# Kernel optimization log

Hardware: AMD Instinct MI355X
Metric: run time of the kernel (lower is better)

## Reference

```python
import jax, jax.numpy as jnp
import numpy as np

B, A, T, D = 4, 64, 128, 512
H = 8
DH = D // H
DFF = 4 * D

def layer_norm(x, g, b, eps=1e-5):
    mu = jnp.mean(x, axis=-1, keepdims=True)
    var = jnp.var(x, axis=-1, keepdims=True)
    return (x - mu) * jax.lax.rsqrt(var + eps) * g + b

def setup_inputs() -> dict:
    key = jax.random.key(0)
    ks = jax.random.split(key, 8)
    s = 0.02
    return {
        "x": jax.random.normal(ks[0], (B, A, T, D), dtype=jnp.float32),
        "ln1_g": jnp.ones((D,), jnp.float32),
        "ln1_b": jnp.zeros((D,), jnp.float32),
        "W_qkv": jax.random.normal(ks[1], (D, 3 * D), jnp.float32) * s,
        "b_qkv": jnp.zeros((3 * D,), jnp.float32),
        "W_proj": jax.random.normal(ks[2], (D, D), jnp.float32) * s,
        "b_proj": jnp.zeros((D,), jnp.float32),
        "ln2_g": jnp.ones((D,), jnp.float32),
        "ln2_b": jnp.zeros((D,), jnp.float32),
        "W_fc": jax.random.normal(ks[3], (D, DFF), jnp.float32) * s,
        "b_fc": jnp.zeros((DFF,), jnp.float32),
        "W_out": jax.random.normal(ks[4], (DFF, D), jnp.float32) * s,
        "b_out": jnp.zeros((D,), jnp.float32),
    }

def reference(x, ln1_g, ln1_b, W_qkv, b_qkv, W_proj, b_proj,
              ln2_g, ln2_b, W_fc, b_fc, W_out, b_out):
    # pre-norm (note: original adds residual from the NORMED x)
    xn = layer_norm(x, ln1_g, ln1_b)
    # qkv projection: [B,A,T,3D]
    qkv = xn @ W_qkv + b_qkv
    q, k, v = jnp.split(qkv, 3, axis=-1)
    # [B,A,T,H,DH]
    q = q.reshape(B, A, T, H, DH)
    k = k.reshape(B, A, T, H, DH)
    v = v.reshape(B, A, T, H, DH)
    # attention across time, per (batch, agent, head): scores [B,A,H,T,T]
    att = jnp.einsum('bathd,bashd->bahts', q, k) * (1.0 / np.sqrt(DH))
    causal = jnp.tril(jnp.ones((T, T), dtype=bool))
    att = jnp.where(causal, att, -jnp.inf)
    att = jax.nn.softmax(att, axis=-1)
    y = jnp.einsum('bahts,bashd->bathd', att, v).reshape(B, A, T, D)
    y = y @ W_proj + b_proj
    x = xn + y
    # MLP block
    xn2 = layer_norm(x, ln2_g, ln2_b)
    h = jax.nn.gelu(xn2 @ W_fc + b_fc, approximate=False)
    m = h @ W_out + b_out
    return xn2 + m
```

## Files before the change

### kernel.cpp

```cpp
#include <hip/hip_runtime.h>
#include <math.h>

#define DEV static __device__ __forceinline__

typedef unsigned short u16;
typedef __attribute__((ext_vector_type(8))) short short8;
typedef __attribute__((ext_vector_type(4))) float floatx4;

DEV u16 f2bf(float f) {
  unsigned u = __float_as_uint(f);
  unsigned r = u + 0x7FFFu + ((u >> 16) & 1u);
  return (u16)(r >> 16);
}
DEV float bf2f(u16 v) { return __uint_as_float(((unsigned)v) << 16); }

typedef __attribute__((address_space(1))) void gvoid;
typedef __attribute__((address_space(3))) void lvoid;

DEV void gload16(const u16* g, u16* l) {
  __builtin_amdgcn_global_load_lds((gvoid*)g, (lvoid*)l, 16, 0, 0);
}

__global__ __launch_bounds__(256) void tcast_k(const float* __restrict__ in,
                                               u16* __restrict__ out, int K, int N) {
  __shared__ float t[32][33];
  int nb = blockIdx.x * 32, kb = blockIdx.y * 32;
  int tx = threadIdx.x, ty = threadIdx.y;
#pragma unroll
  for (int r = 0; r < 32; r += 8)
    t[r + ty][tx] = in[(long)(kb + r + ty) * N + nb + tx];
  __syncthreads();
#pragma unroll
  for (int r = 0; r < 32; r += 8)
    out[(long)(nb + r + ty) * K + kb + tx] = f2bf(t[tx][r + ty]);
}

template <typename TI>
__global__ __launch_bounds__(256) void ln_k(const TI* __restrict__ x,
                                            const float* __restrict__ g,
                                            const float* __restrict__ b,
                                            u16* __restrict__ xb) {
  const int lane = threadIdx.x & 63, wid = threadIdx.x >> 6;
  const long row = (long)blockIdx.x * 4 + wid;
  float vv[8];
  if constexpr (sizeof(TI) == 4) {
    const float4* xr = (const float4*)((const float*)x + row * 512);
    float4 v0 = xr[lane * 2], v1 = xr[lane * 2 + 1];
    vv[0] = v0.x; vv[1] = v0.y; vv[2] = v0.z; vv[3] = v0.w;
    vv[4] = v1.x; vv[5] = v1.y; vv[6] = v1.z; vv[7] = v1.w;
  } else {
    short8 v = *(const short8*)((const u16*)x + row * 512 + lane * 8);
#pragma unroll
    for (int i = 0; i < 8; ++i) vv[i] = bf2f((u16)v[i]);
  }
  float s = 0.f, q = 0.f;
#pragma unroll
  for (int i = 0; i < 8; ++i) { s += vv[i]; q += vv[i] * vv[i]; }
#pragma unroll
  for (int off = 1; off < 64; off <<= 1) {
    s += __shfl_xor(s, off, 64);
    q += __shfl_xor(q, off, 64);
  }
  float mean = s * (1.f / 512.f);
  float var = q * (1.f / 512.f) - mean * mean;
  float rs = rsqrtf(var + 1e-5f);
  const float4* gp = (const float4*)g;
  const float4* bp = (const float4*)b;
  float4 g0 = gp[lane * 2], g1 = gp[lane * 2 + 1];
  float4 b0 = bp[lane * 2], b1 = bp[lane * 2 + 1];
  float gg[8] = {g0.x, g0.y, g0.z, g0.w, g1.x, g1.y, g1.z, g1.w};
  float bb[8] = {b0.x, b0.y, b0.z, b0.w, b1.x, b1.y, b1.z, b1.w};
  short8 ov;
#pragma unroll
  for (int i = 0; i < 8; ++i)
    ov[i] = (short)f2bf((vv[i] - mean) * rs * gg[i] + bb[i]);
  *(short8*)&xb[row * 512 + lane * 8] = ov;
}

template <int EPI>
__global__ __launch_bounds__(256) void gemm_k(const u16* __restrict__ A,
                                              const u16* __restrict__ Bt,
                                              const float* __restrict__ bias,
                                              const u16* __restrict__ res,
                                              void* __restrict__ out,
                                              int M, int N, int K) {
  __shared__ __align__(16) u16 lA[128 * 32];
  __shared__ __align__(16) u16 lB[128 * 32];
  const int tid = threadIdx.x;
  const int lane = tid & 63, wid = tid >> 6;
  const int lane15 = lane & 15, khi = lane >> 4;
  const int wr = wid >> 1, wc = wid & 1;
  const long rowB = (long)blockIdx.y * 128;
  const long colB = (long)blockIdx.x * 128;

  floatx4 acc[4][4];
#pragma unroll
  for (int m = 0; m < 4; ++m)
#pragma unroll
    for (int n = 0; n < 4; ++n) acc[m][n] = floatx4{0.f, 0.f, 0.f, 0.f};

  for (int kt = 0; kt < K; kt += 32) {
    __syncthreads();
#pragma unroll
    for (int j = 0; j < 2; ++j) {
      int c = j * 256 + tid;
      int r = c >> 2, cq = c & 3;
      gload16(A + (rowB + r) * K + kt + cq * 8, &lA[(j * 256 + wid * 64) * 8]);
    }
#pragma unroll
    for (int j = 0; j < 2; ++j) {
      int c = j * 256 + tid;
      int r = c >> 2, cq = c & 3;
      gload16(Bt + (colB + r) * K + kt + cq * 8, &lB[(j * 256 + wid * 64) * 8]);
    }
    asm volatile("s_waitcnt vmcnt(0)" ::: "memory");
    __syncthreads();

    short8 af[4];
#pragma unroll
    for (int m = 0; m < 4; ++m)
      af[m] = *(const short8*)&lA[(wr * 64 + m * 16 + lane15) * 32 + khi * 8];
#pragma unroll
    for (int n = 0; n < 4; ++n) {
      short8 bfg = *(const short8*)&lB[(wc * 64 + n * 16 + lane15) * 32 + khi * 8];
#pragma unroll
      for (int m = 0; m < 4; ++m)
        acc[m][n] = __builtin_amdgcn_mfma_f32_16x16x32_bf16(af[m], bfg, acc[m][n], 0, 0, 0);
    }
  }

  const long r0 = rowB + wr * 64;
  const long c0 = colB + wc * 64;
#pragma unroll
  for (int m = 0; m < 4; ++m) {
#pragma unroll
    for (int n = 0; n < 4; ++n) {
      long col = c0 + n * 16 + lane15;
      float bv = bias[col];
#pragma unroll
      for (int jj = 0; jj < 4; ++jj) {
        long row = r0 + m * 16 + khi * 4 + jj;
        float v = acc[m][n][jj] + bv;
        if (EPI == 1) v = 0.5f * v * (1.f + erff(v * 0.70710678118f));
        if (EPI == 2 || EPI == 3) v += bf2f(res[row * N + col]);
        if (EPI == 3) {
          ((float*)out)[row * N + col] = v;
        } else {
          ((u16*)out)[row * N + col] = f2bf(v);
        }
      }
    }
  }
}

__global__ __launch_bounds__(256) void attn_k(const u16* __restrict__ qkv,
                                              u16* __restrict__ y) {
  union U {
    struct { u16 q[128 * 64]; u16 k[128 * 64]; } qk;
    u16 p[128 * 128];
  };
  __shared__ __align__(16) U u;
  __shared__ __align__(16) u16 vt[64 * 128];

  const int tid = threadIdx.x;
  const int lane = tid & 63, wid = tid >> 6;
  const int lane15 = lane & 15, khi = lane >> 4;
  const int h = blockIdx.x & 7;
  const long R0 = (long)(blockIdx.x >> 3) * 128;
  const u16* base = qkv + R0 * 1536 + h * 64;

#pragma unroll
  for (int it = 0; it < 4; ++it) {
    int c = it * 256 + tid;
    int r = c >> 3, ch = c & 7;
    const u16* gq = base + (long)r * 1536 + ch * 8;
    uint4 dq = *(const uint4*)gq;
    uint4 dk = *(const uint4*)(gq + 512);
    uint4 dv = *(const uint4*)(gq + 1024);
    int qi = (r * 64 + ch * 8) ^ ((r & 7) << 3);
    *(uint4*)&u.qk.q[qi] = dq;
    *(uint4*)&u.qk.k[qi] = dk;
    u16 tmp[8];
    *(uint4*)tmp = dv;
#pragma unroll
    for (int i = 0; i < 8; ++i) {
      int d = ch * 8 + i;
      vt[(d * 128 + r) ^ ((d & 7) << 3)] = tmp[i];
    }
  }
  __syncthreads();

  const int r0 = wid * 32;
  floatx4 sc[2][8];
#pragma unroll
  for (int mt = 0; mt < 2; ++mt)
#pragma unroll
    for (int c = 0; c < 8; ++c) sc[mt][c] = floatx4{0.f, 0.f, 0.f, 0.f};

#pragma unroll
  for (int kk = 0; kk < 2; ++kk) {
    short8 aq[2];
#pragma unroll
    for (int mt = 0; mt < 2; ++mt) {
      int rr = r0 + mt * 16 + lane15;
      aq[mt] = *(const short8*)&u.qk.q[(rr * 64 + kk * 32 + khi * 8) ^ ((rr & 7) << 3)];
    }
#pragma unroll
    for (int c = 0; c < 8; ++c) {
      int rk = c * 16 + lane15;
      short8 bk = *(const short8*)&u.qk.k[(rk * 64 + kk * 32 + khi * 8) ^ ((rk & 7) << 3)];
#pragma unroll
      for (int mt = 0; mt < 2; ++mt)
        sc[mt][c] = __builtin_amdgcn_mfma_f32_16x16x32_bf16(aq[mt], bk, sc[mt][c], 0, 0, 0);
    }
  }
  __syncthreads();

#pragma unroll
  for (int mt = 0; mt < 2; ++mt) {
#pragma unroll
    for (int jj = 0; jj < 4; ++jj) {
      int t = r0 + mt * 16 + khi * 4 + jj;
      float vals[8];
      float mx = -1e30f;
#pragma unroll
      for (int c = 0; c < 8; ++c) {
        int s = c * 16 + lane15;
        float v = sc[mt][c][jj] * 0.125f;
        vals[c] = (s <= t) ? v : -1e30f;
        mx = fmaxf(mx, vals[c]);
      }
#pragma unroll
      for (int off = 1; off < 16; off <<= 1) mx = fmaxf(mx, __shfl_xor(mx, off, 64));
      float sum = 0.f;
#pragma unroll
      for (int c = 0; c < 8; ++c) {
        float p = __expf(vals[c] - mx);
        vals[c] = p;
        sum += p;
      }
#pragma unroll
      for (int off = 1; off < 16; off <<= 1) sum += __shfl_xor(sum, off, 64);
      float inv = 1.f / sum;
#pragma unroll
      for (int c = 0; c < 8; ++c) {
        int s = c * 16 + lane15;
        u.p[(t * 128 + s) ^ ((t & 7) << 3)] = f2bf(vals[c] * inv);
      }
    }
  }
  __syncthreads();

  floatx4 ya[2][4];
#pragma unroll
  for (int mt = 0; mt < 2; ++mt)
#pragma unroll
    for (int n = 0; n < 4; ++n) ya[mt][n] = floatx4{0.f, 0.f, 0.f, 0.f};

#pragma unroll
  for (int kk = 0; kk < 4; ++kk) {
    short8 ap[2];
#pragma unroll
    for (int mt = 0; mt < 2; ++mt) {
      int rr = r0 + mt * 16 + lane15;
      ap[mt] = *(const short8*)&u.p[(rr * 128 + kk * 32 + khi * 8) ^ ((rr & 7) << 3)];
    }
#pragma unroll
    for (int n = 0; n < 4; ++n) {
      int d = n * 16 + lane15;
      short8 bv = *(const short8*)&vt[(d * 128 + kk * 32 + khi * 8) ^ ((d & 7) << 3)];
#pragma unroll
      for (int mt = 0; mt < 2; ++mt)
        ya[mt][n] = __builtin_amdgcn_mfma_f32_16x16x32_bf16(ap[mt], bv, ya[mt][n], 0, 0, 0);
    }
  }

  u16* yb = y + R0 * 512 + h * 64;
#pragma unroll
  for (int mt = 0; mt < 2; ++mt)
#pragma unroll
    for (int n = 0; n < 4; ++n)
#pragma unroll
      for (int jj = 0; jj < 4; ++jj) {
        int t = r0 + mt * 16 + khi * 4 + jj;
        int d = n * 16 + lane15;
        yb[(long)t * 512 + d] = f2bf(ya[mt][n][jj]);
      }
}

extern "C" void kernel_launch(void* const* d_in, const int* in_sizes, int n_in,
                              void* d_out, int out_size, void* d_ws, size_t ws_size,
                              hipStream_t stream) {
  const float* x      = (const float*)d_in[0];
  const float* ln1_g  = (const float*)d_in[1];
  const float* ln1_b  = (const float*)d_in[2];
  const float* W_qkv  = (const float*)d_in[3];
  const float* b_qkv  = (const float*)d_in[4];
  const float* W_proj = (const float*)d_in[5];
  const float* b_proj = (const float*)d_in[6];
  const float* ln2_g  = (const float*)d_in[7];
  const float* ln2_b  = (const float*)d_in[8];
  const float* W_fc   = (const float*)d_in[9];
  const float* b_fc   = (const float*)d_in[10];
  const float* W_out  = (const float*)d_in[11];
  const float* b_out  = (const float*)d_in[12];

  const size_t MiB = 1024 * 1024;
  char* ws = (char*)d_ws;
  u16* wq   = (u16*)(ws + 0);
  u16* wp   = (u16*)(ws + 1536 * 512 * 2);
  u16* wf   = (u16*)(ws + 2 * MiB);
  u16* wo   = (u16*)(ws + 4 * MiB);
  u16* xnB  = (u16*)(ws + 8 * MiB);
  u16* qkvB = (u16*)(ws + 40 * MiB);
  u16* yB   = (u16*)(ws + 136 * MiB);
  u16* x2B  = (u16*)(ws + 40 * MiB);
  u16* xn2B = (u16*)(ws + 8 * MiB);
  u16* hB   = (u16*)(ws + 40 * MiB);

  const int M = 32768;

  tcast_k<<<dim3(1536 / 32, 512 / 32), dim3(32, 8), 0, stream>>>(W_qkv, wq, 512, 1536);
  tcast_k<<<dim3(512 / 32, 512 / 32), dim3(32, 8), 0, stream>>>(W_proj, wp, 512, 512);
  tcast_k<<<dim3(2048 / 32, 512 / 32), dim3(32, 8), 0, stream>>>(W_fc, wf, 512, 2048);
  tcast_k<<<dim3(512 / 32, 2048 / 32), dim3(32, 8), 0, stream>>>(W_out, wo, 2048, 512);

  ln_k<float><<<M / 4, 256, 0, stream>>>(x, ln1_g, ln1_b, xnB);
  gemm_k<0><<<dim3(1536 / 128, M / 128), 256, 0, stream>>>(xnB, wq, b_qkv, nullptr,
                                                           qkvB, M, 1536, 512);
  attn_k<<<2048, 256, 0, stream>>>(qkvB, yB);
  gemm_k<2><<<dim3(512 / 128, M / 128), 256, 0, stream>>>(yB, wp, b_proj, xnB,
                                                          x2B, M, 512, 512);
  ln_k<u16><<<M / 4, 256, 0, stream>>>(x2B, ln2_g, ln2_b, xn2B);
  gemm_k<1><<<dim3(2048 / 128, M / 128), 256, 0, stream>>>(xn2B, wf, b_fc, nullptr,
                                                           hB, M, 2048, 512);
  gemm_k<3><<<dim3(512 / 128, M / 128), 256, 0, stream>>>(hB, wo, b_out, xn2B,
                                                          (float*)d_out, M, 512, 2048);
}
```

Baseline: 532.5 us.

## Fuse LN1 with QKV GEMM and proj+LN2+MLP into one row-block kernel

Replaces the separate layernorm and GEMM launches with two fused kernels. Each block owns 128 rows, holds the normalized activations in a 128 KB LDS tile and streams bf16 weights directly from global memory. In the second kernel, projection, residual, LN2, FC+GELU in 64-column chunks and the output GEMM all run without writing the intermediates x2, xn2 and h to HBM. The trade is that only 256 blocks of 512 threads run, with one block per CU because of the LDS footprint. Weight fragments are also loaded from global memory with no LDS staging or software pipelining, so latency hiding and occupancy may suffer.

```diff
diff --git a/kernel.cpp b/kernel.cpp
--- a/kernel.cpp
+++ b/kernel.cpp
@@ -20,6 +20,13 @@
 DEV void gload16(const u16* g, u16* l) {
   __builtin_amdgcn_global_load_lds((gvoid*)g, (lvoid*)l, 16, 0, 0);
 }
+
+DEV floatx4 mfma16(short8 a, short8 b, floatx4 c) {
+  return __builtin_amdgcn_mfma_f32_16x16x32_bf16(a, b, c, 0, 0, 0);
+}
+
+DEV int aidx(int r, int g) { return r * 512 + ((g ^ (r & 7)) << 3); }
+DEV int hidx(int r, int g) { return (r << 6) + ((g ^ (r & 7)) << 3); }
 
 __global__ __launch_bounds__(256) void tcast_k(const float* __restrict__ in,
                                                u16* __restrict__ out, int K, int N) {
@@ -35,121 +42,87 @@
     out[(long)(nb + r + ty) * K + kb + tx] = f2bf(t[tx][r + ty]);
 }
 
-template <typename TI>
-__global__ __launch_bounds__(256) void ln_k(const TI* __restrict__ x,
-                                            const float* __restrict__ g,
-                                            const float* __restrict__ b,
-                                            u16* __restrict__ xb) {
-  const int lane = threadIdx.x & 63, wid = threadIdx.x >> 6;
-  const long row = (long)blockIdx.x * 4 + wid;
-  float vv[8];
-  if constexpr (sizeof(TI) == 4) {
-    const float4* xr = (const float4*)((const float*)x + row * 512);
-    float4 v0 = xr[lane * 2], v1 = xr[lane * 2 + 1];
-    vv[0] = v0.x; vv[1] = v0.y; vv[2] = v0.z; vv[3] = v0.w;
-    vv[4] = v1.x; vv[5] = v1.y; vv[6] = v1.z; vv[7] = v1.w;
-  } else {
-    short8 v = *(const short8*)((const u16*)x + row * 512 + lane * 8);
-#pragma unroll
-    for (int i = 0; i < 8; ++i) vv[i] = bf2f((u16)v[i]);
-  }
-  float s = 0.f, q = 0.f;
-#pragma unroll
-  for (int i = 0; i < 8; ++i) { s += vv[i]; q += vv[i] * vv[i]; }
-#pragma unroll
-  for (int off = 1; off < 64; off <<= 1) {
-    s += __shfl_xor(s, off, 64);
-    q += __shfl_xor(q, off, 64);
-  }
-  float mean = s * (1.f / 512.f);
-  float var = q * (1.f / 512.f) - mean * mean;
-  float rs = rsqrtf(var + 1e-5f);
-  const float4* gp = (const float4*)g;
-  const float4* bp = (const float4*)b;
-  float4 g0 = gp[lane * 2], g1 = gp[lane * 2 + 1];
-  float4 b0 = bp[lane * 2], b1 = bp[lane * 2 + 1];
-  float gg[8] = {g0.x, g0.y, g0.z, g0.w, g1.x, g1.y, g1.z, g1.w};
-  float bb[8] = {b0.x, b0.y, b0.z, b0.w, b1.x, b1.y, b1.z, b1.w};
-  short8 ov;
-#pragma unroll
-  for (int i = 0; i < 8; ++i)
-    ov[i] = (short)f2bf((vv[i] - mean) * rs * gg[i] + bb[i]);
-  *(short8*)&xb[row * 512 + lane * 8] = ov;
-}
-
-template <int EPI>
-__global__ __launch_bounds__(256) void gemm_k(const u16* __restrict__ A,
-                                              const u16* __restrict__ Bt,
-                                              const float* __restrict__ bias,
-                                              const u16* __restrict__ res,
-                                              void* __restrict__ out,
-                                              int M, int N, int K) {
-  __shared__ __align__(16) u16 lA[128 * 32];
-  __shared__ __align__(16) u16 lB[128 * 32];
+__global__ __launch_bounds__(512) void fusedA_k(const float* __restrict__ x,
+                                                const float* __restrict__ g1,
+                                                const float* __restrict__ b1,
+                                                const u16* __restrict__ wq,
+                                                const float* __restrict__ bq,
+                                                u16* __restrict__ xnB,
+                                                u16* __restrict__ qkvB) {
+  __shared__ __align__(16) u16 as[128 * 512];
   const int tid = threadIdx.x;
-  const int lane = tid & 63, wid = tid >> 6;
+  const int lane = tid & 63, w = tid >> 6;
   const int lane15 = lane & 15, khi = lane >> 4;
-  const int wr = wid >> 1, wc = wid & 1;
-  const long rowB = (long)blockIdx.y * 128;
-  const long colB = (long)blockIdx.x * 128;
-
-  floatx4 acc[4][4];
-#pragma unroll
-  for (int m = 0; m < 4; ++m)
-#pragma unroll
-    for (int n = 0; n < 4; ++n) acc[m][n] = floatx4{0.f, 0.f, 0.f, 0.f};
-
-  for (int kt = 0; kt < K; kt += 32) {
-    __syncthreads();
-#pragma unroll
-    for (int j = 0; j < 2; ++j) {
-      int c = j * 256 + tid;
-      int r = c >> 2, cq = c & 3;
-      gload16(A + (rowB + r) * K + kt + cq * 8, &lA[(j * 256 + wid * 64) * 8]);
-    }
-#pragma unroll
-    for (int j = 0; j < 2; ++j) {
-      int c = j * 256 + tid;
-      int r = c >> 2, cq = c & 3;
-      gload16(Bt + (colB + r) * K + kt + cq * 8, &lB[(j * 256 + wid * 64) * 8]);
-    }
-    asm volatile("s_waitcnt vmcnt(0)" ::: "memory");
-    __syncthreads();
-
-    short8 af[4];
-#pragma unroll
-    for (int m = 0; m < 4; ++m)
-      af[m] = *(const short8*)&lA[(wr * 64 + m * 16 + lane15) * 32 + khi * 8];
-#pragma unroll
-    for (int n = 0; n < 4; ++n) {
-      short8 bfg = *(const short8*)&lB[(wc * 64 + n * 16 + lane15) * 32 + khi * 8];
-#pragma unroll
-      for (int m = 0; m < 4; ++m)
-        acc[m][n] = __builtin_amdgcn_mfma_f32_16x16x32_bf16(af[m], bfg, acc[m][n], 0, 0, 0);
-    }
-  }
-
-  const long r0 = rowB + wr * 64;
-  const long c0 = colB + wc * 64;
-#pragma unroll
-  for (int m = 0; m < 4; ++m) {
-#pragma unroll
-    for (int n = 0; n < 4; ++n) {
-      long col = c0 + n * 16 + lane15;
-      float bv = bias[col];
-#pragma unroll
-      for (int jj = 0; jj < 4; ++jj) {
-        long row = r0 + m * 16 + khi * 4 + jj;
-        float v = acc[m][n][jj] + bv;
-        if (EPI == 1) v = 0.5f * v * (1.f + erff(v * 0.70710678118f));
-        if (EPI == 2 || EPI == 3) v += bf2f(res[row * N + col]);
-        if (EPI == 3) {
-          ((float*)out)[row * N + col] = v;
-        } else {
-          ((u16*)out)[row * N + col] = f2bf(v);
+  const int wr = w >> 2, wcn = w & 3;
+  const long R0 = (long)blockIdx.x * 128;
+
+  {
+    const float4* gp = (const float4*)g1;
+    const float4* bp = (const float4*)b1;
+    float4 gv0 = gp[lane * 2], gv1 = gp[lane * 2 + 1];
+    float4 bv0 = bp[lane * 2], bv1 = bp[lane * 2 + 1];
+    float gg[8] = {gv0.x, gv0.y, gv0.z, gv0.w, gv1.x, gv1.y, gv1.z, gv1.w};
+    float bb[8] = {bv0.x, bv0.y, bv0.z, bv0.w, bv1.x, bv1.y, bv1.z, bv1.w};
+    for (int rr = 0; rr < 16; ++rr) {
+      const int r = w * 16 + rr;
+      const float4* xr = (const float4*)(x + (R0 + r) * 512);
+      float4 v0 = xr[lane * 2], v1 = xr[lane * 2 + 1];
+      float vv[8] = {v0.x, v0.y, v0.z, v0.w, v1.x, v1.y, v1.z, v1.w};
+      float s = 0.f, q = 0.f;
+#pragma unroll
+      for (int i = 0; i < 8; ++i) { s += vv[i]; q += vv[i] * vv[i]; }
+#pragma unroll
+      for (int off = 1; off < 64; off <<= 1) {
+        s += __shfl_xor(s, off, 64);
+        q += __shfl_xor(q, off, 64);
+      }
+      float mean = s * (1.f / 512.f);
+      float var = q * (1.f / 512.f) - mean * mean;
+      float rs = rsqrtf(var + 1e-5f);
+      short8 ov;
+#pragma unroll
+      for (int i = 0; i < 8; ++i)
+        ov[i] = (short)f2bf((vv[i] - mean) * rs * gg[i] + bb[i]);
+      *(short8*)&xnB[(R0 + r) * 512 + lane * 8] = ov;
+      *(short8*)&as[r * 512 + ((lane ^ (r & 7)) << 3)] = ov;
+    }
+  }
+  __syncthreads();
+
+  for (int pass = 0; pass < 3; ++pass) {
+    const int nb0 = pass * 512 + wcn * 128;
+    floatx4 acc[4][8];
+#pragma unroll
+    for (int mt = 0; mt < 4; ++mt)
+#pragma unroll
+      for (int nt = 0; nt < 8; ++nt) acc[mt][nt] = floatx4{0.f, 0.f, 0.f, 0.f};
+#pragma unroll 2
+    for (int ks = 0; ks < 16; ++ks) {
+      short8 bfr[8], afr[4];
+#pragma unroll
+      for (int nt = 0; nt < 8; ++nt)
+        bfr[nt] = *(const short8*)&wq[(long)(nb0 + nt * 16 + lane15) * 512 + ks * 32 + khi * 8];
+#pragma unroll
+      for (int mt = 0; mt < 4; ++mt)
+        afr[mt] = *(const short8*)&as[aidx(wr * 64 + mt * 16 + lane15, ks * 4 + khi)];
+#pragma unroll
+      for (int nt = 0; nt < 8; ++nt)
+#pragma unroll
+        for (int mt = 0; mt < 4; ++mt)
+          acc[mt][nt] = mfma16(afr[mt], bfr[nt], acc[mt][nt]);
+    }
+#pragma unroll
+    for (int mt = 0; mt < 4; ++mt)
+#pragma unroll
+      for (int nt = 0; nt < 8; ++nt) {
+        const int col = nb0 + nt * 16 + lane15;
+        const float bv = bq[col];
+#pragma unroll
+        for (int jj = 0; jj < 4; ++jj) {
+          const int row = wr * 64 + mt * 16 + khi * 4 + jj;
+          qkvB[(R0 + row) * 1536 + col] = f2bf(acc[mt][nt][jj] + bv);
         }
       }
-    }
   }
 }
 
@@ -211,7 +184,7 @@
       short8 bk = *(const short8*)&u.qk.k[(rk * 64 + kk * 32 + khi * 8) ^ ((rk & 7) << 3)];
 #pragma unroll
       for (int mt = 0; mt < 2; ++mt)
-        sc[mt][c] = __builtin_amdgcn_mfma_f32_16x16x32_bf16(aq[mt], bk, sc[mt][c], 0, 0, 0);
+        sc[mt][c] = mfma16(aq[mt], bk, sc[mt][c]);
     }
   }
   __syncthreads();
@@ -271,7 +244,7 @@
       short8 bv = *(const short8*)&vt[(d * 128 + kk * 32 + khi * 8) ^ ((d & 7) << 3)];
 #pragma unroll
       for (int mt = 0; mt < 2; ++mt)
-        ya[mt][n] = __builtin_amdgcn_mfma_f32_16x16x32_bf16(ap[mt], bv, ya[mt][n], 0, 0, 0);
+        ya[mt][n] = mfma16(ap[mt], bv, ya[mt][n]);
     }
   }
 
@@ -286,6 +259,169 @@
         int d = n * 16 + lane15;
         yb[(long)t * 512 + d] = f2bf(ya[mt][n][jj]);
       }
+}
+
+__global__ __launch_bounds__(512) void fusedB_k(const u16* __restrict__ yB,
+                                                const u16* __restrict__ xnB,
+                                                const u16* __restrict__ wp,
+                                                const float* __restrict__ bp,
+                                                const float* __restrict__ g2,
+                                                const float* __restrict__ b2,
+                                                const u16* __restrict__ wf,
+                                                const float* __restrict__ bfc,
+                                                const u16* __restrict__ wo,
+                                                const float* __restrict__ bo,
+                                                float* __restrict__ out) {
+  __shared__ __align__(16) u16 as[128 * 512];
+  __shared__ __align__(16) u16 hs[128 * 64];
+  const int tid = threadIdx.x;
+  const int lane = tid & 63, w = tid >> 6;
+  const int lane15 = lane & 15, khi = lane >> 4;
+  const int wr = w >> 2, wcn = w & 3;
+  const long R0 = (long)blockIdx.x * 128;
+
+  for (int rr = 0; rr < 16; ++rr) {
+    const int r = w * 16 + rr;
+    gload16(yB + (R0 + r) * 512 + ((lane ^ (r & 7)) << 3), &as[r * 512]);
+  }
+  asm volatile("s_waitcnt vmcnt(0)" ::: "memory");
+  __syncthreads();
+
+  floatx4 acc[4][8];
+#pragma unroll
+  for (int mt = 0; mt < 4; ++mt)
+#pragma unroll
+    for (int nt = 0; nt < 8; ++nt) acc[mt][nt] = floatx4{0.f, 0.f, 0.f, 0.f};
+
+#pragma unroll 2
+  for (int ks = 0; ks < 16; ++ks) {
+    short8 bfr[8], afr[4];
+#pragma unroll
+    for (int nt = 0; nt < 8; ++nt)
+      bfr[nt] = *(const short8*)&wp[(long)(wcn * 128 + nt * 16 + lane15) * 512 + ks * 32 + khi * 8];
+#pragma unroll
+    for (int mt = 0; mt < 4; ++mt)
+      afr[mt] = *(const short8*)&as[aidx(wr * 64 + mt * 16 + lane15, ks * 4 + khi)];
+#pragma unroll
+    for (int nt = 0; nt < 8; ++nt)
+#pragma unroll
+      for (int mt = 0; mt < 4; ++mt)
+        acc[mt][nt] = mfma16(afr[mt], bfr[nt], acc[mt][nt]);
+  }
+  __syncthreads();
+
+#pragma unroll
+  for (int mt = 0; mt < 4; ++mt)
+#pragma unroll
+    for (int nt = 0; nt < 8; ++nt) {
+      const int col = wcn * 128 + nt * 16 + lane15;
+      const float bv = bp[col];
+#pragma unroll
+      for (int jj = 0; jj < 4; ++jj) {
+        const int row = wr * 64 + mt * 16 + khi * 4 + jj;
+        float v = acc[mt][nt][jj] + bv + bf2f(xnB[(R0 + row) * 512 + col]);
+        as[row * 512 + (((col >> 3) ^ (row & 7)) << 3) + (col & 7)] = f2bf(v);
+      }
+    }
+  __syncthreads();
+
+  {
+    const float4* gp = (const float4*)g2;
+    const float4* bpx = (const float4*)b2;
+    float4 gv0 = gp[lane * 2], gv1 = gp[lane * 2 + 1];
+    float4 bv0 = bpx[lane * 2], bv1 = bpx[lane * 2 + 1];
+    float gg[8] = {gv0.x, gv0.y, gv0.z, gv0.w, gv1.x, gv1.y, gv1.z, gv1.w};
+    float bb[8] = {bv0.x, bv0.y, bv0.z, bv0.w, bv1.x, bv1.y, bv1.z, bv1.w};
+    for (int rr = 0; rr < 16; ++rr) {
+      const int r = w * 16 + rr;
+      const int idx = r * 512 + ((lane ^ (r & 7)) << 3);
+      short8 v = *(const short8*)&as[idx];
+      float vv[8];
+#pragma unroll
+      for (int i = 0; i < 8; ++i) vv[i] = bf2f((u16)v[i]);
+      float s = 0.f, q = 0.f;
+#pragma unroll
+      for (int i = 0; i < 8; ++i) { s += vv[i]; q += vv[i] * vv[i]; }
+#pragma unroll
+      for (int off = 1; off < 64; off <<= 1) {
+        s += __shfl_xor(s, off, 64);
+        q += __shfl_xor(q, off, 64);
+      }
+      float mean = s * (1.f / 512.f);
+      float var = q * (1.f / 512.f) - mean * mean;
+      float rs = rsqrtf(var + 1e-5f);
+      short8 ov;
+#pragma unroll
+      for (int i = 0; i < 8; ++i)
+        ov[i] = (short)f2bf((vv[i] - mean) * rs * gg[i] + bb[i]);
+      *(short8*)&as[idx] = ov;
+    }
+  }
+  __syncthreads();
+
+#pragma unroll
+  for (int mt = 0; mt < 4; ++mt)
+#pragma unroll
+    for (int nt = 0; nt < 8; ++nt) acc[mt][nt] = floatx4{0.f, 0.f, 0.f, 0.f};
+
+  for (int c = 0; c < 32; ++c) {
+    const int hn0 = c * 64 + wcn * 16;
+    floatx4 hacc[4];
+#pragma unroll
+    for (int mt = 0; mt < 4; ++mt) hacc[mt] = floatx4{0.f, 0.f, 0.f, 0.f};
+#pragma unroll 4
+    for (int ks = 0; ks < 16; ++ks) {
+      short8 bfr = *(const short8*)&wf[(long)(hn0 + lane15) * 512 + ks * 32 + khi * 8];
+#pragma unroll
+      for (int mt = 0; mt < 4; ++mt) {
+        short8 afr = *(const short8*)&as[aidx(wr * 64 + mt * 16 + lane15, ks * 4 + khi)];
+        hacc[mt] = mfma16(afr, bfr, hacc[mt]);
+      }
+    }
+    __syncthreads();
+#pragma unroll
+    for (int mt = 0; mt < 4; ++mt) {
+      const int ccol = wcn * 16 + lane15;
+      const float bv = bfc[c * 64 + ccol];
+#pragma unroll
+      for (int jj = 0; jj < 4; ++jj) {
+        const int row = wr * 64 + mt * 16 + khi * 4 + jj;
+        float v = hacc[mt][jj] + bv;
+        v = 0.5f * v * (1.f + erff(v * 0.70710678118f));
+        hs[(row << 6) + (((ccol >> 3) ^ (row & 7)) << 3) + (ccol & 7)] = f2bf(v);
+      }
+    }
+    __syncthreads();
+#pragma unroll
+    for (int ks2 = 0; ks2 < 2; ++ks2) {
+      short8 bfr[8], afr[4];
+#pragma unroll
+      for (int nt = 0; nt < 8; ++nt)
+        bfr[nt] = *(const short8*)&wo[(long)(wcn * 128 + nt * 16 + lane15) * 2048 + c * 64 + ks2 * 32 + khi * 8];
+#pragma unroll
+      for (int mt = 0; mt < 4; ++mt)
+        afr[mt] = *(const short8*)&hs[hidx(wr * 64 + mt * 16 + lane15, ks2 * 4 + khi)];
+#pragma unroll
+      for (int nt = 0; nt < 8; ++nt)
+#pragma unroll
+        for (int mt = 0; mt < 4; ++mt)
+          acc[mt][nt] = mfma16(afr[mt], bfr[nt], acc[mt][nt]);
+    }
+  }
+
+#pragma unroll
+  for (int mt = 0; mt < 4; ++mt)
+#pragma unroll
+    for (int nt = 0; nt < 8; ++nt) {
+      const int col = wcn * 128 + nt * 16 + lane15;
+      const float bv = bo[col];
+#pragma unroll
+      for (int jj = 0; jj < 4; ++jj) {
+        const int row = wr * 64 + mt * 16 + khi * 4 + jj;
+        float xn2 = bf2f(as[row * 512 + (((col >> 3) ^ (row & 7)) << 3) + (col & 7)]);
+        out[(R0 + row) * 512 + col] = acc[mt][nt][jj] + bv + xn2;
+      }
+    }
 }
 
 extern "C" void kernel_launch(void* const* d_in, const int* in_sizes, int n_in,
@@ -314,26 +450,14 @@
   u16* xnB  = (u16*)(ws + 8 * MiB);
   u16* qkvB = (u16*)(ws + 40 * MiB);
   u16* yB   = (u16*)(ws + 136 * MiB);
-  u16* x2B  = (u16*)(ws + 40 * MiB);
-  u16* xn2B = (u16*)(ws + 8 * MiB);
-  u16* hB   = (u16*)(ws + 40 * MiB);
-
-  const int M = 32768;
 
   tcast_k<<<dim3(1536 / 32, 512 / 32), dim3(32, 8), 0, stream>>>(W_qkv, wq, 512, 1536);
   tcast_k<<<dim3(512 / 32, 512 / 32), dim3(32, 8), 0, stream>>>(W_proj, wp, 512, 512);
   tcast_k<<<dim3(2048 / 32, 512 / 32), dim3(32, 8), 0, stream>>>(W_fc, wf, 512, 2048);
   tcast_k<<<dim3(512 / 32, 2048 / 32), dim3(32, 8), 0, stream>>>(W_out, wo, 2048, 512);
 
-  ln_k<float><<<M / 4, 256, 0, stream>>>(x, ln1_g, ln1_b, xnB);
-  gemm_k<0><<<dim3(1536 / 128, M / 128), 256, 0, stream>>>(xnB, wq, b_qkv, nullptr,
-                                                           qkvB, M, 1536, 512);
+  fusedA_k<<<256, 512, 0, stream>>>(x, ln1_g, ln1_b, wq, b_qkv, xnB, qkvB);
   attn_k<<<2048, 256, 0, stream>>>(qkvB, yB);
-  gemm_k<2><<<dim3(512 / 128, M / 128), 256, 0, stream>>>(yB, wp, b_proj, xnB,
-                                                          x2B, M, 512, 512);
-  ln_k<u16><<<M / 4, 256, 0, stream>>>(x2B, ln2_g, ln2_b, xn2B);
-  gemm_k<1><<<dim3(2048 / 128, M / 128), 256, 0, stream>>>(xn2B, wf, b_fc, nullptr,
-                                                           hB, M, 2048, 512);
-  gemm_k<3><<<dim3(512 / 128, M / 128), 256, 0, stream>>>(hB, wo, b_out, xn2B,
-                                                          (float*)d_out, M, 512, 2048);
-}
+  fusedB_k<<<256, 512, 0, stream>>>(yB, xnB, wp, b_proj, ln2_g, ln2_b,
+                                    wf, b_fc, wo, b_out, (float*)d_out);
+}
```

After: 840.6 us. +57.8%, slower.
